# Optimization experiments

Hardware: AMD Instinct MI355X
Metric: run time of the kernel (lower is better)

## Reference

```python
import jax, jax.numpy as jnp
import numpy as np

LN_EPS = 1e-5

def layer_norm(x, gamma, beta):
    mu = jnp.mean(x, axis=-1, keepdims=True)
    var = jnp.mean(jnp.square(x - mu), axis=-1, keepdims=True)
    return (x - mu) * jax.lax.rsqrt(var + LN_EPS) * gamma + beta

def setup_inputs() -> dict:
    key = jax.random.key(0)
    ks = jax.random.split(key, 10)
    B, C, N = 8, 256, 4096
    s = 1.0 / np.sqrt(C)
    inp = {
        "x": jax.random.normal(ks[0], (B, C, N), dtype=jnp.float32),
        "W_qkv": jax.random.uniform(ks[1], (C, C), jnp.float32, -s, s),            # Linear(dim, dim, bias=False)
        "W_mlp": jax.random.uniform(ks[2], (2 * C, 2 * C), jnp.float32, -0.5 * s, 0.5 * s),
        "b_mlp": jax.random.uniform(ks[3], (2 * C,), jnp.float32, -0.5 * s, 0.5 * s),
        "g1": jnp.ones((4 * C,), jnp.float32),
        "beta1": jnp.zeros((4 * C,), jnp.float32),
        "W_res": jax.random.uniform(ks[4], (C, 4 * C), jnp.float32, -0.25 * s, 0.25 * s),  # Linear(4*dim, dim, bias=False)
        "g2": jnp.ones((C,), jnp.float32),
        "beta2": jnp.zeros((C,), jnp.float32),
    }
    return inp

def reference(x, W_qkv, W_mlp, b_mlp, g1, beta1, W_res, g2, beta2):
    # x: (B, C, N) channels-first -> (B, N, C)
    NITER = 2  # niter_heads
    x = jnp.swapaxes(x, 1, 2)
    x = x @ W_qkv.T                                   # shared_qkv, (B, N, C)
    v = jax.lax.stop_gradient(x)                      # x.clone().detach()
    for _ in range(NITER):
        # first_context = x^T @ v : (B, C, C)
        ctx = jnp.einsum('bnc,bnd->bcd', x, v)
        out = jax.nn.softmax(x, axis=-1) @ ctx        # (B, N, C)
        cat1 = jnp.concatenate([out, v], axis=-1)     # (B, N, 2C)
        mlp = jax.nn.relu(cat1 @ W_mlp.T + b_mlp)     # (B, N, 2C)
        cat2 = jnp.concatenate([cat1, mlp], axis=-1)  # (B, N, 4C)
        # dropout layers are identity in eval mode
        v = layer_norm(cat2, g1, beta1) @ W_res.T + x # residual_mlp + skip
        v = layer_norm(x + v, g2, beta2)
    return jnp.swapaxes(v, 1, 2)                      # back to (B, C, N)
```

## Files before the change

### kernel.cpp

```cpp
#include <hip/hip_runtime.h>
#include <cstdint>
#include <cstddef>


using u16 = unsigned short;
using short8 = __attribute__((ext_vector_type(8))) short;
using bf16x8 = __attribute__((ext_vector_type(8))) __bf16;
using f32x4  = __attribute__((ext_vector_type(4))) float;
using i32x4  = __attribute__((ext_vector_type(4))) int;
using u16x4  = __attribute__((ext_vector_type(4))) u16;
using u16x8  = __attribute__((ext_vector_type(8))) u16;

__device__ __forceinline__ float b2f(u16 u) {
    union { unsigned u32; float f; } c; c.u32 = ((unsigned)u) << 16; return c.f;
}
__device__ __forceinline__ u16 f2b(float f) {
    union { float f; unsigned u; } c; c.f = f;
    unsigned r = c.u + 0x7FFFu + ((c.u >> 16) & 1u);
    return (u16)(r >> 16);
}
__device__ __forceinline__ void cvt(u16 a,  u16& o)   { o = a; }
__device__ __forceinline__ void cvt(float a, u16& o)  { o = f2b(a); }
__device__ __forceinline__ void cvt(float a, float& o){ o = a; }
__device__ __forceinline__ void cvt(u16 a,  float& o) { o = b2f(a); }

__device__ __forceinline__ void glds16(const u16* g, short* l) {
    __builtin_amdgcn_global_load_lds(
        (const __attribute__((address_space(1))) void*)g,
        (__attribute__((address_space(3))) void*)l, 16, 0, 0);
}

template<int MODE, int TRF>
__global__ __launch_bounds__(512)
void gemm_bt(const u16* __restrict__ A, const u16* __restrict__ A2,
             const u16* __restrict__ A3,
             int lda, int lda2, int lda3, int kSplit,
             const u16* __restrict__ B, int ldb, long strA, long strB,
             int statStride, int kChunk, int nKsplit,
             float* __restrict__ outF, u16* __restrict__ outB,
             long sOF, long sOB, int ldo,
             const u16* __restrict__ Xres,
             const float* __restrict__ bias,
             const float2* __restrict__ stats,
             const float* __restrict__ g, const float* __restrict__ be)
{
    __shared__ short lsA[128 * 64];
    __shared__ short lsB[128 * 64];

    const int bz    = blockIdx.z;
    const int batch = bz / nKsplit;
    const int ks    = bz - batch * nKsplit;
    const u16* Ab = A + (size_t)batch * strA;
    const u16* Bb = B + (size_t)batch * strB;
    const int colBase = blockIdx.x * 128;
    const int rowBase = blockIdx.y * 128;
    const int k0 = ks * kChunk;
    const int k1 = k0 + kChunk;

    const int t    = threadIdx.x;
    const int sRow = t >> 3;
    const int sKl  = (t & 7) << 3;
    const int sKg  = (((t & 7) ^ (sRow & 7)) << 3);

    const int lane = t & 63;
    const int w    = t >> 6;
    const int wr   = (w >> 1) * 32;
    const int wc   = (w & 1) * 64;
    const int mrow = lane & 15;
    const int q    = lane >> 4;

    short* ldA0 = &lsA[w * 512];
    short* ldA1 = &lsA[4096 + w * 512];
    short* ldB0 = &lsB[w * 512];
    short* ldB1 = &lsB[4096 + w * 512];

    float2 st0 = {0.f, 0.f}, st1 = {0.f, 0.f};
    if (TRF == 1) {
        const int sb = batch * statStride + rowBase;
        st0 = stats[sb + sRow];
        st1 = stats[sb + sRow + 64];
    }

    auto aPtr = [&](int rloc, int kn) -> const u16* {
        const int arow = rowBase + rloc + sRow;
        if (TRF == 2) {
            if (kn < 256)      return A  + (size_t)arow * lda  + kn + sKg;
            else if (kn < 512) return A2 + (size_t)arow * lda2 + (kn - 256) + sKg;
            else               return A3 + (size_t)arow * lda3 + (kn - 512) + sKg;
        } else if (TRF == 3) {
            if (kn < kSplit)   return Ab + (size_t)arow * lda + kn + sKg;
            return A2 + (size_t)arow * lda2 + (kn - kSplit) + sKg;
        }
        return Ab + (size_t)arow * lda + kn + sKg;
    };
    auto loadX = [&](int rloc, int kn, float2 st) -> i32x4 {
        const int arow = rowBase + rloc + sRow;
        i32x4 raw = *(const i32x4*)(Ab + (size_t)arow * lda + kn + sKg);
        short8 h = __builtin_bit_cast(short8, raw);
        short8 o;
#pragma unroll
        for (int i = 0; i < 8; i++) {
            float v = b2f((u16)h[i]);
            v = __expf(v - st.x) * st.y;
            o[i] = (short)f2b(v);
        }
        return __builtin_bit_cast(i32x4, o);
    };

    const f32x4 fzero = {0.f, 0.f, 0.f, 0.f};
    f32x4 acc[2][4];
#pragma unroll
    for (int i = 0; i < 2; i++)
#pragma unroll
        for (int j = 0; j < 4; j++) acc[i][j] = fzero;

    const u16* pB0 = Bb + (size_t)(colBase + sRow) * ldb + sKg;
    const u16* pB1 = pB0 + (size_t)64 * ldb;
    const u16* pA0 = nullptr; const u16* pA1 = nullptr;
    if (TRF == 0) {
        pA0 = Ab + (size_t)(rowBase + sRow) * lda + sKg;
        pA1 = pA0 + (size_t)64 * lda;
    }

    const int rsw = mrow & 7;
    const int kc0 = (((0 * 4 + q) ^ rsw) << 3);
    const int kc1 = (((1 * 4 + q) ^ rsw) << 3);

    i32x4 a0, a1;
    if (TRF == 1) {
        a0 = loadX(0,  k0, st0);
        a1 = loadX(64, k0, st1);
    }

    for (int kk = k0; kk < k1; kk += 64) {
        if (TRF == 1) {
            *(i32x4*)&lsA[sRow * 64 + sKl]        = a0;
            *(i32x4*)&lsA[(sRow + 64) * 64 + sKl] = a1;
        } else if (TRF == 0) {
            glds16(pA0 + kk, ldA0);
            glds16(pA1 + kk, ldA1);
        } else {
            glds16(aPtr(0,  kk), ldA0);
            glds16(aPtr(64, kk), ldA1);
        }
        glds16(pB0 + kk, ldB0);
        glds16(pB1 + kk, ldB1);
        __syncthreads();
        const int kn = kk + 64;
        if (TRF == 1 && kn < k1) {
            a0 = loadX(0,  kn, st0);
            a1 = loadX(64, kn, st1);
        }
#pragma unroll
        for (int h = 0; h < 2; h++) {
            const int kc = h ? kc1 : kc0;
            bf16x8 af[2], bfr[4];
#pragma unroll
            for (int mi = 0; mi < 2; mi++)
                af[mi] = __builtin_bit_cast(bf16x8,
                    *(const short8*)&lsA[(wr + mi * 16 + mrow) * 64 + kc]);
#pragma unroll
            for (int ni = 0; ni < 4; ni++)
                bfr[ni] = __builtin_bit_cast(bf16x8,
                    *(const short8*)&lsB[(wc + ni * 16 + mrow) * 64 + kc]);
#pragma unroll
            for (int mi = 0; mi < 2; mi++)
#pragma unroll
                for (int ni = 0; ni < 4; ni++)
                    acc[mi][ni] = __builtin_amdgcn_mfma_f32_16x16x32_bf16(
                        af[mi], bfr[ni], acc[mi][ni], 0, 0, 0);
        }
        __syncthreads();
    }

#pragma unroll
    for (int mi = 0; mi < 2; mi++) {
#pragma unroll
        for (int ni = 0; ni < 4; ni++) {
            const int col = colBase + wc + ni * 16 + mrow;
#pragma unroll
            for (int r = 0; r < 4; r++) {
                const int row = rowBase + wr + mi * 16 + q * 4 + r;
                float v = acc[mi][ni][r];
                if (MODE == 0) {
                    outB[(size_t)batch * sOB + (size_t)row * ldo + col] = f2b(v);
                } else if (MODE == 1) {
                    outF[((size_t)batch * nKsplit + ks) * sOF
                         + (size_t)row * ldo + col] = v;
                } else if (MODE == 3) {
                    v += bias[col];
                    v = v > 0.f ? v : 0.f;
                    outB[(size_t)row * ldo + col] = f2b(v);
                } else if (MODE == 4) {
                    const float2 ln = stats[row];
                    v = ln.y * (v - ln.x * g[col]) + be[col]
                        + 2.f * b2f(Xres[(size_t)row * 256 + col]);
                    outB[(size_t)row * ldo + col] = f2b(v);
                }
            }
        }
    }
}

template<typename TIN, typename TOUT>
__global__ __launch_bounds__(256)
void transpose_k(const TIN* __restrict__ in, TOUT* __restrict__ out,
                 int R, int Cc, long sIn, long sOut)
{
    __shared__ TOUT tile[32][33];
    const int b = blockIdx.z;
    const TIN* ib = in + (size_t)b * sIn;
    TOUT* ob = out + (size_t)b * sOut;
    const int c0 = blockIdx.x * 32, r0 = blockIdx.y * 32;
    const int tx = threadIdx.x & 31, ty = threadIdx.x >> 5;
#pragma unroll
    for (int i = 0; i < 32; i += 8)
        cvt(ib[(size_t)(r0 + ty + i) * Cc + c0 + tx], tile[ty + i][tx]);
    __syncthreads();
#pragma unroll
    for (int i = 0; i < 32; i += 8)
        ob[(size_t)(c0 + ty + i) * R + r0 + tx] = tile[tx][ty + i];
}

__global__ __launch_bounds__(256)
void smstats_k(const u16* __restrict__ Xb, float2* __restrict__ st)
{
    const int wave = threadIdx.x >> 6, lane = threadIdx.x & 63;
    const size_t row = (size_t)blockIdx.x * 4 + wave;
    const u16x4 xb = *(const u16x4*)(Xb + row * 256 + lane * 4);
    const float x0 = b2f(xb.x), x1 = b2f(xb.y), x2 = b2f(xb.z), x3 = b2f(xb.w);
    float m = fmaxf(fmaxf(x0, x1), fmaxf(x2, x3));
    for (int o = 32; o > 0; o >>= 1) m = fmaxf(m, __shfl_xor(m, o));
    float s = __expf(x0 - m) + __expf(x1 - m) + __expf(x2 - m) + __expf(x3 - m);
    for (int o = 32; o > 0; o >>= 1) s += __shfl_xor(s, o);
    if (lane == 0) st[row] = make_float2(m, 1.f / s);
}

__global__ __launch_bounds__(256)
void stats1024_k(const u16* __restrict__ OUT, const u16* __restrict__ V,
                 const u16* __restrict__ MLPo, float2* __restrict__ st)
{
    const int wave = threadIdx.x >> 6, lane = threadIdx.x & 63;
    const size_t row = (size_t)blockIdx.x * 4 + wave;
    const int c = lane * 16;
    const u16* src;
    if (c < 256)       src = OUT  + row * 256 + c;
    else if (c < 512)  src = V    + row * 256 + (c - 256);
    else               src = MLPo + row * 512 + (c - 512);
    short8 r0 = *(const short8*)(src);
    short8 r1 = *(const short8*)(src + 8);
    float s = 0.f, s2 = 0.f;
#pragma unroll
    for (int i = 0; i < 8; i++) {
        const float a = b2f((u16)r0[i]), b = b2f((u16)r1[i]);
        s += a + b; s2 += a * a + b * b;
    }
    for (int o = 32; o > 0; o >>= 1) { s += __shfl_xor(s, o); s2 += __shfl_xor(s2, o); }
    const float mean = s * (1.f / 1024.f);
    const float var  = s2 * (1.f / 1024.f) - mean * mean;
    if (lane == 0) st[row] = make_float2(mean, rsqrtf(var + 1e-5f));
}

template<typename OUTT, bool WRITE_VB>
__global__ __launch_bounds__(256)
void ln256t_k(const u16* __restrict__ Tb, const float* __restrict__ g,
              const float* __restrict__ be, u16* __restrict__ Vb,
              OUTT* __restrict__ outT)
{
    constexpr int STRIDE = (sizeof(OUTT) == 2) ? 266 : 261;
    __shared__ OUTT tile[32 * STRIDE];
    const int wid = threadIdx.x >> 6, lane = threadIdx.x & 63;
    const int bx = blockIdx.x;
    const size_t r0 = (size_t)bx * 32;
    const int b  = bx >> 7;
    const int n0 = (bx & 127) * 32;

#pragma unroll
    for (int j = 0; j < 8; j++) {
        const int lr = wid * 8 + j;
        const size_t row = r0 + lr;
        const u16x4 tb = *(const u16x4*)(Tb + row * 256 + lane * 4);
        const float x0 = b2f(tb.x), x1 = b2f(tb.y), x2 = b2f(tb.z), x3 = b2f(tb.w);
        float s  = x0 + x1 + x2 + x3;
        float s2 = x0 * x0 + x1 * x1 + x2 * x2 + x3 * x3;
        for (int o = 32; o > 0; o >>= 1) { s += __shfl_xor(s, o); s2 += __shfl_xor(s2, o); }
        const float mean = s * (1.f / 256.f);
        const float var  = s2 * (1.f / 256.f) - mean * mean;
        const float rstd = rsqrtf(var + 1e-5f);
        const int c = lane * 4;
        float4 ov = { (x0 - mean) * rstd * g[c + 0] + be[c + 0],
                      (x1 - mean) * rstd * g[c + 1] + be[c + 1],
                      (x2 - mean) * rstd * g[c + 2] + be[c + 2],
                      (x3 - mean) * rstd * g[c + 3] + be[c + 3] };
        if (WRITE_VB) {
            u16x4 vb = { f2b(ov.x), f2b(ov.y), f2b(ov.z), f2b(ov.w) };
            *(u16x4*)(Vb + row * 256 + c) = vb;
        }
        OUTT* tl = &tile[lr * STRIDE + c];
        cvt(ov.x, tl[0]); cvt(ov.y, tl[1]); cvt(ov.z, tl[2]); cvt(ov.w, tl[3]);
    }
    __syncthreads();

    const int c = threadIdx.x;
    OUTT* dst = outT + ((size_t)b * 256 + c) * 4096 + n0;
    if (sizeof(OUTT) == 2) {
#pragma unroll
        for (int k = 0; k < 4; k++) {
            u16x8 v;
#pragma unroll
            for (int i = 0; i < 8; i++) v[i] = *(const u16*)&tile[(k * 8 + i) * STRIDE + c];
            *(u16x8*)((u16*)dst + k * 8) = v;
        }
    } else {
#pragma unroll
        for (int k = 0; k < 8; k++) {
            float4 v;
            v.x = *(const float*)&tile[(k * 4 + 0) * STRIDE + c];
            v.y = *(const float*)&tile[(k * 4 + 1) * STRIDE + c];
            v.z = *(const float*)&tile[(k * 4 + 2) * STRIDE + c];
            v.w = *(const float*)&tile[(k * 4 + 3) * STRIDE + c];
            *(float4*)((float*)dst + k * 4) = v;
        }
    }
}

__global__ __launch_bounds__(256)
void ctxreduce_k(const float* __restrict__ ctxp, u16* __restrict__ ctxb)
{
    const int i = blockIdx.x * 256 + threadIdx.x;
    const int batch  = i >> 14;
    const int within = i & 16383;
    const float4* src = (const float4*)ctxp + (size_t)batch * 16 * 16384 + within;
    float4 s = {0.f, 0.f, 0.f, 0.f};
#pragma unroll
    for (int ks = 0; ks < 16; ks++) {
        const float4 v = src[(size_t)ks * 16384];
        s.x += v.x; s.y += v.y; s.z += v.z; s.w += v.w;
    }
    u16x4 o = { f2b(s.x), f2b(s.y), f2b(s.z), f2b(s.w) };
    ((u16x4*)ctxb)[i] = o;
}

__global__ __launch_bounds__(256)
void wconv_k(const float* __restrict__ Wq, const float* __restrict__ Wm,
             u16* __restrict__ oq, u16* __restrict__ om)
{
    const int i = blockIdx.x * 256 + threadIdx.x;
    const float* src; u16* dst; int j;
    if (i < 16384) { src = Wq; dst = oq; j = i; }
    else           { src = Wm; dst = om; j = i - 16384; }
    const float4 v = ((const float4*)src)[j];
    u16x4 o = { f2b(v.x), f2b(v.y), f2b(v.z), f2b(v.w) };
    ((u16x4*)dst)[j] = o;
}

__global__ __launch_bounds__(256)
void wresprep_k(const float* __restrict__ Wres, const float* __restrict__ g1,
                const float* __restrict__ be1, u16* __restrict__ Wr_b,
                float* __restrict__ sg, float* __restrict__ br)
{
    const int wv = threadIdx.x >> 6, lane = threadIdx.x & 63;
    const int row = blockIdx.x * 4 + wv;
    const float* src = Wres + (size_t)row * 1024;
    float s = 0.f, b = 0.f;
#pragma unroll
    for (int j = 0; j < 4; j++) {
        const int c = j * 256 + lane * 4;
        const float4 w  = *(const float4*)(src + c);
        const float4 gg = *(const float4*)(g1 + c);
        const float4 bb = *(const float4*)(be1 + c);
        const float4 wg = { w.x * gg.x, w.y * gg.y, w.z * gg.z, w.w * gg.w };
        u16x4 o = { f2b(wg.x), f2b(wg.y), f2b(wg.z), f2b(wg.w) };
        *(u16x4*)(Wr_b + (size_t)row * 1024 + c) = o;
        s += wg.x + wg.y + wg.z + wg.w;
        b += w.x * bb.x + w.y * bb.y + w.z * bb.z + w.w * bb.w;
    }
    for (int o = 32; o > 0; o >>= 1) { s += __shfl_xor(s, o); b += __shfl_xor(b, o); }
    if (lane == 0) { sg[row] = s; br[row] = b; }
}

extern "C" void kernel_launch(void* const* d_in, const int* in_sizes, int n_in,
                              void* d_out, int out_size, void* d_ws, size_t ws_size,
                              hipStream_t stream)
{
    (void)in_sizes; (void)n_in; (void)out_size; (void)ws_size;
    const float* x    = (const float*)d_in[0];
    const float* Wqkv = (const float*)d_in[1];
    const float* Wmlp = (const float*)d_in[2];
    const float* bmlp = (const float*)d_in[3];
    const float* g1   = (const float*)d_in[4];
    const float* be1  = (const float*)d_in[5];
    const float* Wres = (const float*)d_in[6];
    const float* g2   = (const float*)d_in[7];
    const float* be2  = (const float*)d_in[8];

    char* ws = (char*)d_ws;
    u16*    Xb   = (u16*)ws;    ws += (size_t)16777216;
    u16*    XT   = (u16*)ws;    ws += (size_t)16777216;
    u16*    Vb   = (u16*)ws;    ws += (size_t)16777216;
    u16*    VT2  = (u16*)ws;    ws += (size_t)16777216;
    u16*    OUT  = (u16*)ws;    ws += (size_t)16777216;
    u16*    MLPo = (u16*)ws;    ws += (size_t)33554432;
    u16*    Tb   = (u16*)ws;    ws += (size_t)16777216;
    float*  ctxp = (float*)ws;  ws += (size_t)33554432;
    u16*    ctxb = (u16*)ws;    ws += (size_t)1048576;
    float2* smst = (float2*)ws; ws += (size_t)262144;
    float2* lnst = (float2*)ws; ws += (size_t)262144;
    u16*    Wq_b = (u16*)ws;    ws += (size_t)131072;
    u16*    Wm_b = (u16*)ws;    ws += (size_t)524288;
    u16*    Wr_b = (u16*)ws;    ws += (size_t)524288;
    float*  sg   = (float*)ws;  ws += (size_t)1024;
    float*  br   = (float*)ws;  ws += (size_t)1024;
    u16*    xt   = MLPo;

    wconv_k<<<dim3(320), 256, 0, stream>>>(Wqkv, Wmlp, Wq_b, Wm_b);
    wresprep_k<<<dim3(64), 256, 0, stream>>>(Wres, g1, be1, Wr_b, sg, br);

    transpose_k<float, u16><<<dim3(128, 8, 8), 256, 0, stream>>>(
        x, xt, 256, 4096, 256L * 4096, 4096L * 256);

    gemm_bt<0, 0><<<dim3(2, 256, 1), 512, 0, stream>>>(
        xt, nullptr, nullptr, 256, 0, 0, 0, Wq_b, 256, 0, 0, 0, 256, 1,
        nullptr, Xb, 0, 0, 256, nullptr, nullptr, nullptr, nullptr, nullptr);

    smstats_k<<<dim3(8192), 256, 0, stream>>>(Xb, smst);

    transpose_k<u16, u16><<<dim3(8, 128, 8), 256, 0, stream>>>(
        Xb, XT, 4096, 256, 4096L * 256, 256L * 4096);

    const u16* VTcur = XT;
    const u16* Vcur  = Xb;

    for (int it = 0; it < 2; ++it) {
        gemm_bt<1, 0><<<dim3(2, 2, 128), 512, 0, stream>>>(
            VTcur, nullptr, nullptr, 4096, 0, 0, 0, XT, 4096,
            1048576, 1048576, 0, 256, 16,
            ctxp, nullptr, 65536, 0, 256, nullptr, nullptr, nullptr, nullptr, nullptr);
        ctxreduce_k<<<dim3(512), 256, 0, stream>>>(ctxp, ctxb);

        gemm_bt<0, 1><<<dim3(2, 32, 8), 512, 0, stream>>>(
            Xb, nullptr, nullptr, 256, 0, 0, 0, ctxb, 256,
            1048576, 65536, 4096, 256, 1,
            nullptr, OUT, 0, 1048576, 256, nullptr, nullptr, smst, nullptr, nullptr);

        gemm_bt<3, 3><<<dim3(4, 256, 1), 512, 0, stream>>>(
            OUT, Vcur, nullptr, 256, 256, 0, 256, Wm_b, 512, 0, 0, 0, 512, 1,
            nullptr, MLPo, 0, 0, 512, nullptr, bmlp, nullptr, nullptr, nullptr);

        stats1024_k<<<dim3(8192), 256, 0, stream>>>(OUT, Vcur, MLPo, lnst);

        gemm_bt<4, 2><<<dim3(2, 256, 1), 512, 0, stream>>>(
            OUT, Vcur, MLPo, 256, 256, 512, 0, Wr_b, 1024, 0, 0, 0, 1024, 1,
            nullptr, Tb, 0, 0, 256, Xb, nullptr, lnst, sg, br);

        if (it == 0) {
            ln256t_k<u16, true><<<dim3(1024), 256, 0, stream>>>(
                Tb, g2, be2, Vb, VT2);
            VTcur = VT2;
            Vcur  = Vb;
        } else {
            ln256t_k<float, false><<<dim3(1024), 256, 0, stream>>>(
                Tb, g2, be2, nullptr, (float*)d_out);
        }
    }
}
```

Measured before the change: 362.7 us.

## Double-buffer LDS tiles in gemm_bt to overlap global loads with MFMA

Splits the shared-memory A and B tiles into two buffers so the next K-tile is loaded into one buffer while MFMAs run on the other. This drops one barrier per iteration. For the softmax-transform path, the raw loads are issued early and the exp transform is applied after the MFMAs. LDS use doubles to 64KB per block, which can lower occupancy.

```diff
diff --git a/kernel.cpp b/kernel.cpp
--- a/kernel.cpp
+++ b/kernel.cpp
@@ -44,8 +44,8 @@
              const float2* __restrict__ stats,
              const float* __restrict__ g, const float* __restrict__ be)
 {
-    __shared__ short lsA[128 * 64];
-    __shared__ short lsB[128 * 64];
+    __shared__ short lsA[2][128 * 64];
+    __shared__ short lsB[2][128 * 64];
 
     const int bz    = blockIdx.z;
     const int batch = bz / nKsplit;
@@ -69,11 +69,6 @@
     const int mrow = lane & 15;
     const int q    = lane >> 4;
 
-    short* ldA0 = &lsA[w * 512];
-    short* ldA1 = &lsA[4096 + w * 512];
-    short* ldB0 = &lsB[w * 512];
-    short* ldB1 = &lsB[4096 + w * 512];
-
     float2 st0 = {0.f, 0.f}, st1 = {0.f, 0.f};
     if (TRF == 1) {
         const int sb = batch * statStride + rowBase;
@@ -93,9 +88,11 @@
         }
         return Ab + (size_t)arow * lda + kn + sKg;
     };
-    auto loadX = [&](int rloc, int kn, float2 st) -> i32x4 {
+    auto rawA = [&](int rloc, int kn) -> i32x4 {
         const int arow = rowBase + rloc + sRow;
-        i32x4 raw = *(const i32x4*)(Ab + (size_t)arow * lda + kn + sKg);
+        return *(const i32x4*)(Ab + (size_t)arow * lda + kn + sKg);
+    };
+    auto xf = [&](i32x4 raw, float2 st) -> i32x4 {
         short8 h = __builtin_bit_cast(short8, raw);
         short8 o;
 #pragma unroll
@@ -126,30 +123,44 @@
     const int kc0 = (((0 * 4 + q) ^ rsw) << 3);
     const int kc1 = (((1 * 4 + q) ^ rsw) << 3);
 
-    i32x4 a0, a1;
+    auto stageB = [&](int buf, int kk) {
+        glds16(pB0 + kk, &lsB[buf][w * 512]);
+        glds16(pB1 + kk, &lsB[buf][4096 + w * 512]);
+    };
+    auto stageA = [&](int buf, int kk) {
+        if (TRF == 0) {
+            glds16(pA0 + kk, &lsA[buf][w * 512]);
+            glds16(pA1 + kk, &lsA[buf][4096 + w * 512]);
+        } else {
+            glds16(aPtr(0,  kk), &lsA[buf][w * 512]);
+            glds16(aPtr(64, kk), &lsA[buf][4096 + w * 512]);
+        }
+    };
+
+    i32x4 ra0, ra1;
     if (TRF == 1) {
-        a0 = loadX(0,  k0, st0);
-        a1 = loadX(64, k0, st1);
-    }
-
+        ra0 = rawA(0, k0); ra1 = rawA(64, k0);
+        *(i32x4*)&lsA[0][sRow * 64 + sKl]        = xf(ra0, st0);
+        *(i32x4*)&lsA[0][(sRow + 64) * 64 + sKl] = xf(ra1, st1);
+        stageB(0, k0);
+    } else {
+        stageA(0, k0);
+        stageB(0, k0);
+    }
+    __syncthreads();
+
+    int cur = 0;
     for (int kk = k0; kk < k1; kk += 64) {
-        if (TRF == 1) {
-            *(i32x4*)&lsA[sRow * 64 + sKl]        = a0;
-            *(i32x4*)&lsA[(sRow + 64) * 64 + sKl] = a1;
-        } else if (TRF == 0) {
-            glds16(pA0 + kk, ldA0);
-            glds16(pA1 + kk, ldA1);
-        } else {
-            glds16(aPtr(0,  kk), ldA0);
-            glds16(aPtr(64, kk), ldA1);
-        }
-        glds16(pB0 + kk, ldB0);
-        glds16(pB1 + kk, ldB1);
-        __syncthreads();
         const int kn = kk + 64;
-        if (TRF == 1 && kn < k1) {
-            a0 = loadX(0,  kn, st0);
-            a1 = loadX(64, kn, st1);
+        const bool more = kn < k1;
+        if (more) {
+            if (TRF == 1) {
+                ra0 = rawA(0, kn); ra1 = rawA(64, kn);
+                stageB(cur ^ 1, kn);
+            } else {
+                stageA(cur ^ 1, kn);
+                stageB(cur ^ 1, kn);
+            }
         }
 #pragma unroll
         for (int h = 0; h < 2; h++) {
@@ -158,11 +169,11 @@
 #pragma unroll
             for (int mi = 0; mi < 2; mi++)
                 af[mi] = __builtin_bit_cast(bf16x8,
-                    *(const short8*)&lsA[(wr + mi * 16 + mrow) * 64 + kc]);
+                    *(const short8*)&lsA[cur][(wr + mi * 16 + mrow) * 64 + kc]);
 #pragma unroll
             for (int ni = 0; ni < 4; ni++)
                 bfr[ni] = __builtin_bit_cast(bf16x8,
-                    *(const short8*)&lsB[(wc + ni * 16 + mrow) * 64 + kc]);
+                    *(const short8*)&lsB[cur][(wc + ni * 16 + mrow) * 64 + kc]);
 #pragma unroll
             for (int mi = 0; mi < 2; mi++)
 #pragma unroll
@@ -170,7 +181,14 @@
                     acc[mi][ni] = __builtin_amdgcn_mfma_f32_16x16x32_bf16(
                         af[mi], bfr[ni], acc[mi][ni], 0, 0, 0);
         }
-        __syncthreads();
+        if (more) {
+            if (TRF == 1) {
+                *(i32x4*)&lsA[cur ^ 1][sRow * 64 + sKl]        = xf(ra0, st0);
+                *(i32x4*)&lsA[cur ^ 1][(sRow + 64) * 64 + sKl] = xf(ra1, st1);
+            }
+            __syncthreads();
+            cur ^= 1;
+        }
     }
 
 #pragma unroll
```

Result: no change. 366.9 us (+1.2%).

## Stage two 64-wide K slices per barrier pair in GEMM main loop

Applied to the files above, without the earlier changes.

The GEMM main loop now loads two consecutive 64-wide K chunks into doubled LDS buffers before each barrier and computes both, so each iteration covers 128 of K. This halves the number of __syncthreads pairs per K range. For the softmax-transform path it prefetches raw global data for two chunks and moves the exp/scale transform to the LDS store. It doubles LDS use to 64 KB per block, which may reduce occupancy, and it assumes kChunk is a multiple of 128.

```diff
diff --git a/kernel.cpp b/kernel.cpp
--- a/kernel.cpp
+++ b/kernel.cpp
@@ -44,8 +44,8 @@
              const float2* __restrict__ stats,
              const float* __restrict__ g, const float* __restrict__ be)
 {
-    __shared__ short lsA[128 * 64];
-    __shared__ short lsB[128 * 64];
+    __shared__ short lsA[2][8192];
+    __shared__ short lsB[2][8192];
 
     const int bz    = blockIdx.z;
     const int batch = bz / nKsplit;
@@ -69,11 +69,6 @@
     const int mrow = lane & 15;
     const int q    = lane >> 4;
 
-    short* ldA0 = &lsA[w * 512];
-    short* ldA1 = &lsA[4096 + w * 512];
-    short* ldB0 = &lsB[w * 512];
-    short* ldB1 = &lsB[4096 + w * 512];
-
     float2 st0 = {0.f, 0.f}, st1 = {0.f, 0.f};
     if (TRF == 1) {
         const int sb = batch * statStride + rowBase;
@@ -93,9 +88,11 @@
         }
         return Ab + (size_t)arow * lda + kn + sKg;
     };
-    auto loadX = [&](int rloc, int kn, float2 st) -> i32x4 {
+    auto rawA = [&](int rloc, int kn) -> i32x4 {
         const int arow = rowBase + rloc + sRow;
-        i32x4 raw = *(const i32x4*)(Ab + (size_t)arow * lda + kn + sKg);
+        return *(const i32x4*)(Ab + (size_t)arow * lda + kn + sKg);
+    };
+    auto xf = [&](i32x4 raw, float2 st) -> i32x4 {
         short8 h = __builtin_bit_cast(short8, raw);
         short8 o;
 #pragma unroll
@@ -126,31 +123,17 @@
     const int kc0 = (((0 * 4 + q) ^ rsw) << 3);
     const int kc1 = (((1 * 4 + q) ^ rsw) << 3);
 
-    i32x4 a0, a1;
-    if (TRF == 1) {
-        a0 = loadX(0,  k0, st0);
-        a1 = loadX(64, k0, st1);
-    }
-
-    for (int kk = k0; kk < k1; kk += 64) {
-        if (TRF == 1) {
-            *(i32x4*)&lsA[sRow * 64 + sKl]        = a0;
-            *(i32x4*)&lsA[(sRow + 64) * 64 + sKl] = a1;
-        } else if (TRF == 0) {
-            glds16(pA0 + kk, ldA0);
-            glds16(pA1 + kk, ldA1);
-        } else {
-            glds16(aPtr(0,  kk), ldA0);
-            glds16(aPtr(64, kk), ldA1);
-        }
-        glds16(pB0 + kk, ldB0);
-        glds16(pB1 + kk, ldB1);
-        __syncthreads();
-        const int kn = kk + 64;
-        if (TRF == 1 && kn < k1) {
-            a0 = loadX(0,  kn, st0);
-            a1 = loadX(64, kn, st1);
-        }
+    auto stageA1 = [&](int half, int kk) {
+        short* d0 = &lsA[half][w * 512];
+        short* d1 = &lsA[half][4096 + w * 512];
+        if (TRF == 0) { glds16(pA0 + kk, d0); glds16(pA1 + kk, d1); }
+        else          { glds16(aPtr(0, kk), d0); glds16(aPtr(64, kk), d1); }
+    };
+    auto stageB1 = [&](int half, int kk) {
+        glds16(pB0 + kk, &lsB[half][w * 512]);
+        glds16(pB1 + kk, &lsB[half][4096 + w * 512]);
+    };
+    auto compute = [&](int half) {
 #pragma unroll
         for (int h = 0; h < 2; h++) {
             const int kc = h ? kc1 : kc0;
@@ -158,11 +141,11 @@
 #pragma unroll
             for (int mi = 0; mi < 2; mi++)
                 af[mi] = __builtin_bit_cast(bf16x8,
-                    *(const short8*)&lsA[(wr + mi * 16 + mrow) * 64 + kc]);
+                    *(const short8*)&lsA[half][(wr + mi * 16 + mrow) * 64 + kc]);
 #pragma unroll
             for (int ni = 0; ni < 4; ni++)
                 bfr[ni] = __builtin_bit_cast(bf16x8,
-                    *(const short8*)&lsB[(wc + ni * 16 + mrow) * 64 + kc]);
+                    *(const short8*)&lsB[half][(wc + ni * 16 + mrow) * 64 + kc]);
 #pragma unroll
             for (int mi = 0; mi < 2; mi++)
 #pragma unroll
@@ -170,6 +153,34 @@
                     acc[mi][ni] = __builtin_amdgcn_mfma_f32_16x16x32_bf16(
                         af[mi], bfr[ni], acc[mi][ni], 0, 0, 0);
         }
+    };
+
+    i32x4 a00, a10, a01, a11;
+    if (TRF == 1) {
+        a00 = rawA(0, k0);      a10 = rawA(64, k0);
+        a01 = rawA(0, k0 + 64); a11 = rawA(64, k0 + 64);
+    }
+
+    for (int kk = k0; kk < k1; kk += 128) {
+        if (TRF == 1) {
+            *(i32x4*)&lsA[0][sRow * 64 + sKl]        = xf(a00, st0);
+            *(i32x4*)&lsA[0][(sRow + 64) * 64 + sKl] = xf(a10, st1);
+            *(i32x4*)&lsA[1][sRow * 64 + sKl]        = xf(a01, st0);
+            *(i32x4*)&lsA[1][(sRow + 64) * 64 + sKl] = xf(a11, st1);
+        } else {
+            stageA1(0, kk);
+            stageA1(1, kk + 64);
+        }
+        stageB1(0, kk);
+        stageB1(1, kk + 64);
+        __syncthreads();
+        const int kn = kk + 128;
+        if (TRF == 1 && kn < k1) {
+            a00 = rawA(0, kn);      a10 = rawA(64, kn);
+            a01 = rawA(0, kn + 64); a11 = rawA(64, kn + 64);
+        }
+        compute(0);
+        compute(1);
         __syncthreads();
     }
 
```

After: 374.7 us. 3.3% more time.

## Fuse softmax stats and transpose into QKV GEMM epilogue

Applied to the files above, without the earlier changes.

The QKV projection GEMM epilogue now writes both the row-major bf16 output and its transposed copy, and accumulates per-row exp sums into the softmax stats through atomics. This removes the separate softmax-stats kernel and the bf16 transpose kernel, at the cost of a small zeroing kernel and atomic traffic. Softmax now skips max subtraction (m=0) and the consumer takes the reciprocal of the sum, which risks overflow for large activations. The transposed stores are 4-element strided writes, so they may coalesce poorly.

```diff
diff --git a/kernel.cpp b/kernel.cpp
--- a/kernel.cpp
+++ b/kernel.cpp
@@ -77,8 +77,10 @@
     float2 st0 = {0.f, 0.f}, st1 = {0.f, 0.f};
     if (TRF == 1) {
         const int sb = batch * statStride + rowBase;
-        st0 = stats[sb + sRow];
-        st1 = stats[sb + sRow + 64];
+        const float2 t0 = stats[sb + sRow];
+        const float2 t1 = stats[sb + sRow + 64];
+        st0 = make_float2(0.f, 1.f / t0.y);
+        st1 = make_float2(0.f, 1.f / t1.y);
     }
 
     auto aPtr = [&](int rloc, int kn) -> const u16* {
@@ -171,6 +173,41 @@
                         af[mi], bfr[ni], acc[mi][ni], 0, 0, 0);
         }
         __syncthreads();
+    }
+
+    if (MODE == 5) {
+        u16* XT = const_cast<u16*>(Xres);
+        float2* sm = const_cast<float2*>(stats);
+        float rsum[2][4] = {{0.f,0.f,0.f,0.f},{0.f,0.f,0.f,0.f}};
+#pragma unroll
+        for (int mi = 0; mi < 2; mi++) {
+#pragma unroll
+            for (int ni = 0; ni < 4; ni++) {
+                const int col  = colBase + wc + ni * 16 + mrow;
+                const int row0 = rowBase + wr + mi * 16 + q * 4;
+                u16x4 hv;
+#pragma unroll
+                for (int r = 0; r < 4; r++) {
+                    const u16 h = f2b(acc[mi][ni][r]);
+                    hv[r] = h;
+                    outB[(size_t)(row0 + r) * ldo + col] = h;
+                    rsum[mi][r] += __expf(b2f(h));
+                }
+                *(u16x4*)(XT + (size_t)(row0 >> 12) * 1048576
+                             + (size_t)col * 4096 + (row0 & 4095)) = hv;
+            }
+        }
+#pragma unroll
+        for (int mi = 0; mi < 2; mi++)
+#pragma unroll
+            for (int r = 0; r < 4; r++) {
+                float s = rsum[mi][r];
+                s += __shfl_xor(s, 1); s += __shfl_xor(s, 2);
+                s += __shfl_xor(s, 4); s += __shfl_xor(s, 8);
+                if (mrow == 0)
+                    atomicAdd(&sm[rowBase + wr + mi * 16 + q * 4 + r].y, s);
+            }
+        return;
     }
 
 #pragma unroll
@@ -223,17 +260,9 @@
 }
 
 __global__ __launch_bounds__(256)
-void smstats_k(const u16* __restrict__ Xb, float2* __restrict__ st)
-{
-    const int wave = threadIdx.x >> 6, lane = threadIdx.x & 63;
-    const size_t row = (size_t)blockIdx.x * 4 + wave;
-    const u16x4 xb = *(const u16x4*)(Xb + row * 256 + lane * 4);
-    const float x0 = b2f(xb.x), x1 = b2f(xb.y), x2 = b2f(xb.z), x3 = b2f(xb.w);
-    float m = fmaxf(fmaxf(x0, x1), fmaxf(x2, x3));
-    for (int o = 32; o > 0; o >>= 1) m = fmaxf(m, __shfl_xor(m, o));
-    float s = __expf(x0 - m) + __expf(x1 - m) + __expf(x2 - m) + __expf(x3 - m);
-    for (int o = 32; o > 0; o >>= 1) s += __shfl_xor(s, o);
-    if (lane == 0) st[row] = make_float2(m, 1.f / s);
+void zerosm_k(float2* __restrict__ p)
+{
+    p[blockIdx.x * 256 + threadIdx.x] = make_float2(0.f, 0.f);
 }
 
 __global__ __launch_bounds__(256)
@@ -415,18 +444,14 @@
 
     wconv_k<<<dim3(320), 256, 0, stream>>>(Wqkv, Wmlp, Wq_b, Wm_b);
     wresprep_k<<<dim3(64), 256, 0, stream>>>(Wres, g1, be1, Wr_b, sg, br);
+    zerosm_k<<<dim3(128), 256, 0, stream>>>(smst);
 
     transpose_k<float, u16><<<dim3(128, 8, 8), 256, 0, stream>>>(
         x, xt, 256, 4096, 256L * 4096, 4096L * 256);
 
-    gemm_bt<0, 0><<<dim3(2, 256, 1), 512, 0, stream>>>(
+    gemm_bt<5, 0><<<dim3(2, 256, 1), 512, 0, stream>>>(
         xt, nullptr, nullptr, 256, 0, 0, 0, Wq_b, 256, 0, 0, 0, 256, 1,
-        nullptr, Xb, 0, 0, 256, nullptr, nullptr, nullptr, nullptr, nullptr);
-
-    smstats_k<<<dim3(8192), 256, 0, stream>>>(Xb, smst);
-
-    transpose_k<u16, u16><<<dim3(8, 128, 8), 256, 0, stream>>>(
-        Xb, XT, 4096, 256, 4096L * 256, 256L * 4096);
+        nullptr, Xb, 0, 0, 256, XT, nullptr, smst, nullptr, nullptr);
 
     const u16* VTcur = XT;
     const u16* Vcur  = Xb;
```

After: 355.4 us. -2.0%, faster.
